# Performance work log

Measured on AMD Instinct MI355X. Metric: run time of the kernel, lower is better.

The kernel has to match this reference:

```python
import jax, jax.numpy as jnp
import numpy as np

D_MODEL = 1024
NUM_HEADS = 16
HEAD_DIM = D_MODEL // NUM_HEADS
WINDOW = 256
NEG = -1000000000.0


def setup_inputs() -> dict:
    key = jax.random.key(0)
    ks = jax.random.split(key, 9)
    B, N, D = 2, 2048, D_MODEL
    s = 1.0 / np.sqrt(D)
    inp = {
        "x": jax.random.normal(ks[0], (B, N, D), dtype=jnp.float32),
        "Wq": jax.random.normal(ks[1], (D, D), dtype=jnp.float32) * s,
        "bq": jnp.zeros((D,), dtype=jnp.float32),
        "Wk": jax.random.normal(ks[2], (D, D), dtype=jnp.float32) * s,
        "bk": jnp.zeros((D,), dtype=jnp.float32),
        "Wv": jax.random.normal(ks[3], (D, D), dtype=jnp.float32) * s,
        "bv": jnp.zeros((D,), dtype=jnp.float32),
        "Wo": jax.random.normal(ks[4], (D, D), dtype=jnp.float32) * s,
        "bo": jnp.zeros((D,), dtype=jnp.float32),
    }
    return inp


def reference(x, Wq, bq, Wk, bk, Wv, bv, Wo, bo):
    B, N, D = x.shape
    H, hd = NUM_HEADS, HEAD_DIM
    q = (x @ Wq + bq).reshape(B, N, H, hd).transpose(0, 2, 1, 3)  # [B,H,N,hd]
    k = (x @ Wk + bk).reshape(B, N, H, hd).transpose(0, 2, 1, 3)
    v = (x @ Wv + bv).reshape(B, N, H, hd).transpose(0, 2, 1, 3)

    i = jnp.arange(N)[:, None]
    j = jnp.arange(N)[None, :]
    blocked = (j > i) | (j < i - WINDOW)  # causal + local window
    mask = jnp.where(blocked, jnp.float32(NEG), jnp.float32(0.0))  # [N,N]

    logits = jnp.einsum("bhid,bhjd->bhij", q, k) / jnp.sqrt(jnp.float32(hd))
    logits = logits + mask[None, None, :, :]
    attn = jax.nn.softmax(logits, axis=-1)
    out = jnp.einsum("bhij,bhjd->bhid", attn, v)  # [B,H,N,hd]
    out = out.transpose(0, 2, 1, 3).reshape(B, N, D)
    return out @ Wo + bo
```

## Files before the change

### kernel.cpp

```cpp
#include <hip/hip_runtime.h>


typedef unsigned short ushort_t;
typedef __bf16 bf16x8 __attribute__((ext_vector_type(8)));
typedef float f32x4 __attribute__((ext_vector_type(4)));
typedef unsigned short ushort8 __attribute__((ext_vector_type(8)));

#define LOG2E 1.4426950408889634f

static __device__ __forceinline__ ushort_t f2b(float f) {
    union { float f; unsigned int u; } x;
    x.f = f;
    unsigned int u = x.u;
    unsigned int r = (u + 0x7FFFu + ((u >> 16) & 1u)) >> 16;
    return (ushort_t)r;
}

static __device__ __forceinline__ void store_out(float* p, float v) { *p = v; }
static __device__ __forceinline__ void store_out(ushort_t* p, float v) { *p = f2b(v); }

static __device__ __forceinline__ void gload_lds16(const ushort_t* g, ushort_t* l) {
    __builtin_amdgcn_global_load_lds(
        (const __attribute__((address_space(1))) void*)g,
        (__attribute__((address_space(3))) void*)l, 16, 0, 0);
}

__global__ __launch_bounds__(256) void cast_f32_bf16_kernel(
    const float* __restrict__ in, ushort_t* __restrict__ out) {
    int i = (blockIdx.x * 256 + threadIdx.x) * 8;
    f32x4 a = *(const f32x4*)&in[i];
    f32x4 b = *(const f32x4*)&in[i + 4];
    ushort8 o;
#pragma unroll
    for (int e = 0; e < 4; e++) o[e] = f2b(a[e]);
#pragma unroll
    for (int e = 0; e < 4; e++) o[4 + e] = f2b(b[e]);
    *(ushort8*)&out[i] = o;
}

__global__ __launch_bounds__(256) void transpose_cast_kernel(
    const float* __restrict__ W0, const float* __restrict__ W1,
    const float* __restrict__ W2, const float* __restrict__ W3,
    ushort_t* __restrict__ T0, ushort_t* __restrict__ T1,
    ushort_t* __restrict__ T2, ushort_t* __restrict__ T3) {
    __shared__ ushort_t tile[32][33];
    const float* W;
    ushort_t* T;
    switch (blockIdx.z) {
        case 0: W = W0; T = T0; break;
        case 1: W = W1; T = T1; break;
        case 2: W = W2; T = T2; break;
        default: W = W3; T = T3; break;
    }
    int tx = threadIdx.x, ty = threadIdx.y;
    int x = blockIdx.x * 32 + tx;
    int ybase = blockIdx.y * 32 + ty;
#pragma unroll
    for (int r = 0; r < 4; r++) tile[ty + r * 8][tx] = f2b(W[(ybase + r * 8) * 1024 + x]);
    __syncthreads();
    int xo = blockIdx.y * 32 + tx;
    int yobase = blockIdx.x * 32 + ty;
#pragma unroll
    for (int r = 0; r < 4; r++) T[(yobase + r * 8) * 1024 + xo] = tile[tx][ty + r * 8];
}

template <typename OutT, int MODE>
__global__ __launch_bounds__(256) void gemm_bt_kernel(
    const ushort_t* __restrict__ A,
    const ushort_t* __restrict__ Bt0, const ushort_t* __restrict__ Bt1,
    const ushort_t* __restrict__ Bt2,
    const float* __restrict__ bias0, const float* __restrict__ bias1,
    const float* __restrict__ bias2,
    OutT* __restrict__ C0, OutT* __restrict__ C1, OutT* __restrict__ C2,
    float os0, float os1, float os2) {
    __shared__ ushort_t Al[64 * 64];
    __shared__ ushort_t Bl[128 * 64];

    const int id = blockIdx.x;
    const int xcd = id & 7;
    const int s = id >> 3;
    int m_blk, ncol, zsel;
    if (MODE == 0) {
        m_blk = (xcd >> 1) * 16 + (s & 15);
        ncol = (xcd & 1) * 12 + (s >> 4);
        zsel = ncol >> 3;
        ncol &= 7;
    } else {
        m_blk = xcd * 8 + (s & 7);
        ncol = s >> 3;
        zsel = 0;
    }
    const int m0 = m_blk * 64;
    const int n0 = ncol * 128;

    const ushort_t* Bt;
    const float* bias;
    OutT* C;
    float oscale;
    if (zsel == 0) { Bt = Bt0; bias = bias0; C = C0; oscale = os0; }
    else if (zsel == 1) { Bt = Bt1; bias = bias1; C = C1; oscale = os1; }
    else { Bt = Bt2; bias = bias2; C = C2; oscale = os2; }

    const int tid = threadIdx.x;
    const int w = tid >> 6;
    const int l = tid & 63;
    const int wm = (w >> 1) * 32;
    const int wn = (w & 1) * 64;
    const int lrow = l & 15;
    const int lq = l >> 4;

    f32x4 acc[2][4];
#pragma unroll
    for (int mi = 0; mi < 2; mi++)
#pragma unroll
        for (int ni = 0; ni < 4; ni++) acc[mi][ni] = 0.0f;

    for (int kt = 0; kt < 1024; kt += 64) {
#pragma unroll
        for (int t = 0; t < 2; t++) {
            int idx = t * 256 + tid;
            gload_lds16(&A[(long)(m0 + (idx >> 3)) * 1024 + kt + (idx & 7) * 8], &Al[idx * 8]);
        }
#pragma unroll
        for (int t = 0; t < 4; t++) {
            int idx = t * 256 + tid;
            gload_lds16(&Bt[(long)(n0 + (idx >> 3)) * 1024 + kt + (idx & 7) * 8], &Bl[idx * 8]);
        }
        __syncthreads();
#pragma unroll
        for (int ks = 0; ks < 64; ks += 32) {
            bf16x8 af[2], bfr[4];
#pragma unroll
            for (int mi = 0; mi < 2; mi++)
                af[mi] = *(const bf16x8*)&Al[(wm + mi * 16 + lrow) * 64 + ks + lq * 8];
#pragma unroll
            for (int ni = 0; ni < 4; ni++)
                bfr[ni] = *(const bf16x8*)&Bl[(wn + ni * 16 + lrow) * 64 + ks + lq * 8];
#pragma unroll
            for (int mi = 0; mi < 2; mi++)
#pragma unroll
                for (int ni = 0; ni < 4; ni++)
                    acc[mi][ni] = __builtin_amdgcn_mfma_f32_16x16x32_bf16(
                        af[mi], bfr[ni], acc[mi][ni], 0, 0, 0);
        }
        __syncthreads();
    }

#pragma unroll
    for (int ni = 0; ni < 4; ni++) {
        int n = n0 + wn + ni * 16 + lrow;
        float bv = bias[n];
#pragma unroll
        for (int mi = 0; mi < 2; mi++) {
#pragma unroll
            for (int r = 0; r < 4; r++) {
                int m = m0 + wm + mi * 16 + lq * 4 + r;
                store_out(&C[(long)m * 1024 + n], (acc[mi][ni][r] + bv) * oscale);
            }
        }
    }
}

__global__ __launch_bounds__(256) void attn_kernel(
    const ushort_t* __restrict__ Q, const ushort_t* __restrict__ K,
    const ushort_t* __restrict__ V, ushort_t* __restrict__ O) {
    __shared__ ushort_t Kl[128 * 64];
    __shared__ ushort_t Vt[64 * 136];
    __shared__ ushort_t Pb[4 * 16 * 40];

    const int id = blockIdx.x;
    const int xcd = id & 7;
    const int s = id >> 3;
    const int bh = xcd * 4 + (s >> 5);
    const int b = bh >> 4;
    const int h = bh & 15;
    const int i0 = (s & 31) * 64;

    const int tid = threadIdx.x;
    const int w = tid >> 6;
    const int l = tid & 63;
    const int lrow = l & 15;
    const int lq = l >> 4;
    const int q0 = i0 + w * 16;

    const long baseBH = ((long)b * 2048) * 1024 + (long)h * 64;

    const ushort_t* qrow = Q + baseBH + (long)(q0 + lrow) * 1024;
    bf16x8 aq0 = *(const bf16x8*)&qrow[lq * 8];
    bf16x8 aq1 = *(const bf16x8*)&qrow[32 + lq * 8];

    float lpart[4];
    f32x4 oacc[4];
#pragma unroll
    for (int r = 0; r < 4; r++) lpart[r] = 0.0f;
#pragma unroll
    for (int ni = 0; ni < 4; ni++) oacc[ni] = 0.0f;

    const int kstart = (i0 - 256) > 0 ? (i0 - 256) : 0;
    const int kend = i0 + 64;
    ushort_t* Pw = &Pb[w * 16 * 40];

    for (int cs = kstart; cs < kend; cs += 128) {
        const int ce = (cs + 128 < kend) ? cs + 128 : kend;
        const int rows = ce - cs;
#pragma unroll
        for (int t = 0; t < 4; t++) {
            int idx = t * 256 + tid;
            int rr = idx >> 3;
            int cc = (idx & 7) * 8;
            if (rr < rows)
                *(ushort8*)&Kl[idx * 8] = *(const ushort8*)&K[baseBH + (long)(cs + rr) * 1024 + cc];
        }
        {
            int rr = tid >> 1;
            int ch = (tid & 1) * 32;
            if (rr < rows) {
                const ushort_t* vrow = V + baseBH + (long)(cs + rr) * 1024 + ch;
#pragma unroll
                for (int g = 0; g < 4; g++) {
                    ushort8 vv = *(const ushort8*)&vrow[g * 8];
#pragma unroll
                    for (int e = 0; e < 8; e++) Vt[(ch + g * 8 + e) * 136 + rr] = vv[e];
                }
            }
        }
        __syncthreads();

        for (int kb = cs; kb < ce; kb += 32) {
            if (kb > q0 + 15 || kb + 31 < q0 - 256) continue;
            const int rb = kb - cs;
            f32x4 S0 = 0.0f, S1 = 0.0f;
            {
                bf16x8 bk;
                bk = *(const bf16x8*)&Kl[(rb + lrow) * 64 + lq * 8];
                S0 = __builtin_amdgcn_mfma_f32_16x16x32_bf16(aq0, bk, S0, 0, 0, 0);
                bk = *(const bf16x8*)&Kl[(rb + lrow) * 64 + 32 + lq * 8];
                S0 = __builtin_amdgcn_mfma_f32_16x16x32_bf16(aq1, bk, S0, 0, 0, 0);
                bk = *(const bf16x8*)&Kl[(rb + 16 + lrow) * 64 + lq * 8];
                S1 = __builtin_amdgcn_mfma_f32_16x16x32_bf16(aq0, bk, S1, 0, 0, 0);
                bk = *(const bf16x8*)&Kl[(rb + 16 + lrow) * 64 + 32 + lq * 8];
                S1 = __builtin_amdgcn_mfma_f32_16x16x32_bf16(aq1, bk, S1, 0, 0, 0);
            }
            const int col0 = kb + lrow;
            const int col1 = kb + 16 + lrow;
#pragma unroll
            for (int r = 0; r < 4; r++) {
                const int i = q0 + lq * 4 + r;
                float p0 = (col0 > i || col0 < i - 256) ? 0.0f : exp2f(S0[r] * LOG2E);
                float p1 = (col1 > i || col1 < i - 256) ? 0.0f : exp2f(S1[r] * LOG2E);
                lpart[r] += p0 + p1;
                const int prow = lq * 4 + r;
                Pw[prow * 40 + lrow] = f2b(p0);
                Pw[prow * 40 + 16 + lrow] = f2b(p1);
            }
            bf16x8 pf = *(const bf16x8*)&Pw[lrow * 40 + lq * 8];
#pragma unroll
            for (int ni = 0; ni < 4; ni++) {
                bf16x8 vf = *(const bf16x8*)&Vt[(ni * 16 + lrow) * 136 + rb + lq * 8];
                oacc[ni] = __builtin_amdgcn_mfma_f32_16x16x32_bf16(pf, vf, oacc[ni], 0, 0, 0);
            }
        }
        __syncthreads();
    }

    float lS[4];
#pragma unroll
    for (int r = 0; r < 4; r++) {
        float rs = lpart[r];
#pragma unroll
        for (int off = 8; off; off >>= 1) rs += __shfl_xor(rs, off, 64);
        lS[r] = rs;
    }

#pragma unroll
    for (int ni = 0; ni < 4; ni++) {
#pragma unroll
        for (int r = 0; r < 4; r++) {
            const int i = q0 + lq * 4 + r;
            const int d = ni * 16 + lrow;
            O[baseBH + (long)i * 1024 + d] = f2b(oacc[ni][r] / lS[r]);
        }
    }
}

extern "C" void kernel_launch(void* const* d_in, const int* in_sizes, int n_in,
                              void* d_out, int out_size, void* d_ws, size_t ws_size,
                              hipStream_t stream) {
    const float* x  = (const float*)d_in[0];
    const float* Wq = (const float*)d_in[1];
    const float* bq = (const float*)d_in[2];
    const float* Wk = (const float*)d_in[3];
    const float* bk = (const float*)d_in[4];
    const float* Wv = (const float*)d_in[5];
    const float* bv = (const float*)d_in[6];
    const float* Wo = (const float*)d_in[7];
    const float* bo = (const float*)d_in[8];
    float* out = (float*)d_out;

    ushort_t* ws = (ushort_t*)d_ws;
    const size_t WMAT = (size_t)1024 * 1024;
    const size_t ACT = (size_t)2 * 2048 * 1024;
    ushort_t* xbf = ws;
    ushort_t* Wqt = xbf + ACT;
    ushort_t* Wkt = Wqt + WMAT;
    ushort_t* Wvt = Wkt + WMAT;
    ushort_t* Wot = Wvt + WMAT;
    ushort_t* qws = Wot + WMAT;
    ushort_t* kws = qws + ACT;
    ushort_t* vws = kws + ACT;
    ushort_t* aws = xbf;

    cast_f32_bf16_kernel<<<dim3((unsigned)(ACT / 2048)), 256, 0, stream>>>(x, xbf);

    transpose_cast_kernel<<<dim3(32, 32, 4), dim3(32, 8), 0, stream>>>(
        Wq, Wk, Wv, Wo, Wqt, Wkt, Wvt, Wot);

    gemm_bt_kernel<ushort_t, 0><<<1536, 256, 0, stream>>>(
        xbf, Wqt, Wkt, Wvt, bq, bk, bv, qws, kws, vws, 0.125f, 1.0f, 1.0f);

    attn_kernel<<<1024, 256, 0, stream>>>(qws, kws, vws, aws);

    gemm_bt_kernel<float, 1><<<512, 256, 0, stream>>>(
        aws, Wot, Wot, Wot, bo, bo, bo, out, out, out, 1.0f, 1.0f, 1.0f);
}
```

Measured before the change: 178.9 us.

## Write V pre-transposed from QKV GEMM and enlarge QKV GEMM M-tile

The QKV projection GEMM now stores V in a per-head transposed layout [b,h,d,n], so the attention kernel can fill its V^T shared tile with vectorized row loads instead of scalar transposing stores. K loads in attention switch to direct global-to-LDS loads, with clamped indices replacing the bounds checks. The QKV GEMM M tile doubles to 128 rows (MF=4, 768 blocks), raising per-block reuse of B at the cost of more accumulator registers and fewer blocks. The transposed V store is strided in global memory, which may make the GEMM epilogue writes less coalesced.

```diff
diff --git a/kernel.cpp b/kernel.cpp
--- a/kernel.cpp
+++ b/kernel.cpp
@@ -64,7 +64,7 @@
     for (int r = 0; r < 4; r++) T[(yobase + r * 8) * 1024 + xo] = tile[tx][ty + r * 8];
 }
 
-template <typename OutT, int MODE>
+template <typename OutT, int MODE, int MF>
 __global__ __launch_bounds__(256) void gemm_bt_kernel(
     const ushort_t* __restrict__ A,
     const ushort_t* __restrict__ Bt0, const ushort_t* __restrict__ Bt1,
@@ -73,7 +73,7 @@
     const float* __restrict__ bias2,
     OutT* __restrict__ C0, OutT* __restrict__ C1, OutT* __restrict__ C2,
     float os0, float os1, float os2) {
-    __shared__ ushort_t Al[64 * 64];
+    __shared__ ushort_t Al[MF * 32 * 64];
     __shared__ ushort_t Bl[128 * 64];
 
     const int id = blockIdx.x;
@@ -81,8 +81,8 @@
     const int s = id >> 3;
     int m_blk, ncol, zsel;
     if (MODE == 0) {
-        m_blk = (xcd >> 1) * 16 + (s & 15);
-        ncol = (xcd & 1) * 12 + (s >> 4);
+        m_blk = (xcd >> 1) * 8 + (s & 7);
+        ncol = (xcd & 1) * 12 + (s >> 3);
         zsel = ncol >> 3;
         ncol &= 7;
     } else {
@@ -90,7 +90,7 @@
         ncol = s >> 3;
         zsel = 0;
     }
-    const int m0 = m_blk * 64;
+    const int m0 = m_blk * (MF * 32);
     const int n0 = ncol * 128;
 
     const ushort_t* Bt;
@@ -104,20 +104,20 @@
     const int tid = threadIdx.x;
     const int w = tid >> 6;
     const int l = tid & 63;
-    const int wm = (w >> 1) * 32;
+    const int wm = (w >> 1) * (MF * 16);
     const int wn = (w & 1) * 64;
     const int lrow = l & 15;
     const int lq = l >> 4;
 
-    f32x4 acc[2][4];
-#pragma unroll
-    for (int mi = 0; mi < 2; mi++)
+    f32x4 acc[MF][4];
+#pragma unroll
+    for (int mi = 0; mi < MF; mi++)
 #pragma unroll
         for (int ni = 0; ni < 4; ni++) acc[mi][ni] = 0.0f;
 
     for (int kt = 0; kt < 1024; kt += 64) {
 #pragma unroll
-        for (int t = 0; t < 2; t++) {
+        for (int t = 0; t < MF; t++) {
             int idx = t * 256 + tid;
             gload_lds16(&A[(long)(m0 + (idx >> 3)) * 1024 + kt + (idx & 7) * 8], &Al[idx * 8]);
         }
@@ -129,15 +129,15 @@
         __syncthreads();
 #pragma unroll
         for (int ks = 0; ks < 64; ks += 32) {
-            bf16x8 af[2], bfr[4];
-#pragma unroll
-            for (int mi = 0; mi < 2; mi++)
+            bf16x8 af[MF], bfr[4];
+#pragma unroll
+            for (int mi = 0; mi < MF; mi++)
                 af[mi] = *(const bf16x8*)&Al[(wm + mi * 16 + lrow) * 64 + ks + lq * 8];
 #pragma unroll
             for (int ni = 0; ni < 4; ni++)
                 bfr[ni] = *(const bf16x8*)&Bl[(wn + ni * 16 + lrow) * 64 + ks + lq * 8];
 #pragma unroll
-            for (int mi = 0; mi < 2; mi++)
+            for (int mi = 0; mi < MF; mi++)
 #pragma unroll
                 for (int ni = 0; ni < 4; ni++)
                     acc[mi][ni] = __builtin_amdgcn_mfma_f32_16x16x32_bf16(
@@ -146,16 +146,34 @@
         __syncthreads();
     }
 
-#pragma unroll
-    for (int ni = 0; ni < 4; ni++) {
-        int n = n0 + wn + ni * 16 + lrow;
-        float bv = bias[n];
-#pragma unroll
-        for (int mi = 0; mi < 2; mi++) {
-#pragma unroll
-            for (int r = 0; r < 4; r++) {
-                int m = m0 + wm + mi * 16 + lq * 4 + r;
-                store_out(&C[(long)m * 1024 + n], (acc[mi][ni][r] + bv) * oscale);
+    if (MODE == 0 && zsel == 2) {
+#pragma unroll
+        for (int ni = 0; ni < 4; ni++) {
+            int n = n0 + wn + ni * 16 + lrow;
+            int h = n >> 6, d = n & 63;
+            float bv = bias[n];
+#pragma unroll
+            for (int mi = 0; mi < MF; mi++) {
+#pragma unroll
+                for (int r = 0; r < 4; r++) {
+                    int m = m0 + wm + mi * 16 + lq * 4 + r;
+                    long dst = ((long)(((m >> 11) << 4) + h) * 64 + d) * 2048 + (m & 2047);
+                    store_out(&C[dst], acc[mi][ni][r] + bv);
+                }
+            }
+        }
+    } else {
+#pragma unroll
+        for (int ni = 0; ni < 4; ni++) {
+            int n = n0 + wn + ni * 16 + lrow;
+            float bv = bias[n];
+#pragma unroll
+            for (int mi = 0; mi < MF; mi++) {
+#pragma unroll
+                for (int r = 0; r < 4; r++) {
+                    int m = m0 + wm + mi * 16 + lq * 4 + r;
+                    store_out(&C[(long)m * 1024 + n], (acc[mi][ni][r] + bv) * oscale);
+                }
             }
         }
     }
@@ -163,7 +181,7 @@
 
 __global__ __launch_bounds__(256) void attn_kernel(
     const ushort_t* __restrict__ Q, const ushort_t* __restrict__ K,
-    const ushort_t* __restrict__ V, ushort_t* __restrict__ O) {
+    const ushort_t* __restrict__ VT, ushort_t* __restrict__ O) {
     __shared__ ushort_t Kl[128 * 64];
     __shared__ ushort_t Vt[64 * 136];
     __shared__ ushort_t Pb[4 * 16 * 40];
@@ -184,6 +202,7 @@
     const int q0 = i0 + w * 16;
 
     const long baseBH = ((long)b * 2048) * 1024 + (long)h * 64;
+    const long baseVT = (long)bh * 64 * 2048;
 
     const ushort_t* qrow = Q + baseBH + (long)(q0 + lrow) * 1024;
     bf16x8 aq0 = *(const bf16x8*)&qrow[lq * 8];
@@ -201,31 +220,26 @@
     ushort_t* Pw = &Pb[w * 16 * 40];
 
     for (int cs = kstart; cs < kend; cs += 128) {
-        const int ce = (cs + 128 < kend) ? cs + 128 : kend;
-        const int rows = ce - cs;
 #pragma unroll
         for (int t = 0; t < 4; t++) {
             int idx = t * 256 + tid;
-            int rr = idx >> 3;
-            int cc = (idx & 7) * 8;
-            if (rr < rows)
-                *(ushort8*)&Kl[idx * 8] = *(const ushort8*)&K[baseBH + (long)(cs + rr) * 1024 + cc];
-        }
-        {
-            int rr = tid >> 1;
-            int ch = (tid & 1) * 32;
-            if (rr < rows) {
-                const ushort_t* vrow = V + baseBH + (long)(cs + rr) * 1024 + ch;
-#pragma unroll
-                for (int g = 0; g < 4; g++) {
-                    ushort8 vv = *(const ushort8*)&vrow[g * 8];
-#pragma unroll
-                    for (int e = 0; e < 8; e++) Vt[(ch + g * 8 + e) * 136 + rr] = vv[e];
-                }
-            }
+            int key = cs + (idx >> 3);
+            key = key < 2047 ? key : 2047;
+            gload_lds16(&K[baseBH + (long)key * 1024 + (idx & 7) * 8], &Kl[idx * 8]);
+        }
+#pragma unroll
+        for (int j = 0; j < 4; j++) {
+            int idx = j * 256 + tid;
+            int d = idx >> 4;
+            int kk = (idx & 15) * 8;
+            int key = cs + kk;
+            key = key <= 2040 ? key : 2040;
+            ushort8 vv = *(const ushort8*)&VT[baseVT + (long)d * 2048 + key];
+            *(ushort8*)&Vt[d * 136 + kk] = vv;
         }
         __syncthreads();
 
+        const int ce = (cs + 128 < kend) ? cs + 128 : kend;
         for (int kb = cs; kb < ce; kb += 32) {
             if (kb > q0 + 15 || kb + 31 < q0 - 256) continue;
             const int rb = kb - cs;
@@ -307,7 +321,7 @@
     ushort_t* Wot = Wvt + WMAT;
     ushort_t* qws = Wot + WMAT;
     ushort_t* kws = qws + ACT;
-    ushort_t* vws = kws + ACT;
+    ushort_t* vtws = kws + ACT;
     ushort_t* aws = xbf;
 
     cast_f32_bf16_kernel<<<dim3((unsigned)(ACT / 2048)), 256, 0, stream>>>(x, xbf);
@@ -315,11 +329,11 @@
     transpose_cast_kernel<<<dim3(32, 32, 4), dim3(32, 8), 0, stream>>>(
         Wq, Wk, Wv, Wo, Wqt, Wkt, Wvt, Wot);
 
-    gemm_bt_kernel<ushort_t, 0><<<1536, 256, 0, stream>>>(
-        xbf, Wqt, Wkt, Wvt, bq, bk, bv, qws, kws, vws, 0.125f, 1.0f, 1.0f);
-
-    attn_kernel<<<1024, 256, 0, stream>>>(qws, kws, vws, aws);
-
-    gemm_bt_kernel<float, 1><<<512, 256, 0, stream>>>(
+    gemm_bt_kernel<ushort_t, 0, 4><<<768, 256, 0, stream>>>(
+        xbf, Wqt, Wkt, Wvt, bq, bk, bv, qws, kws, vtws, 0.125f, 1.0f, 1.0f);
+
+    attn_kernel<<<1024, 256, 0, stream>>>(qws, kws, vtws, aws);
+
+    gemm_bt_kernel<float, 1, 2><<<512, 256, 0, stream>>>(
         aws, Wot, Wot, Wot, bo, bo, bo, out, out, out, 1.0f, 1.0f, 1.0f);
 }
```

Result: slower. 198.2 us (+10.8%).
